# Kernel tuning notes

Hardware: AMD Instinct MI355X
Metric: run time of the kernel (lower is better)

## Reference

```python
import jax, jax.numpy as jnp
import numpy as np

M1, M2 = 20, 20  # retained DCT modes per layer

def dct1_last(x):
    # scipy.fftpack unnormalized DCT-I along last axis via FFT of even extension
    N = x.shape[-1]
    ext = jnp.concatenate([x, x[..., -2:0:-1]], axis=-1)  # length 2N-2
    return jnp.fft.rfft(ext).real[..., :N]

def dct1_2d(x):
    x = dct1_last(x)                       # along axis -1
    x = dct1_last(x.swapaxes(-1, -2)).swapaxes(-1, -2)  # along axis -2
    return x

def setup_inputs() -> dict:
    key = jax.random.key(0)
    ks = jax.random.split(key, 11)
    B, X, Y, Din, C, FC, Dout, L = 8, 256, 256, 3, 64, 128, 1, 3
    scale = 1.0 / (C * C)
    return {
        "x": jax.random.normal(ks[0], (B, X, Y, Din), jnp.float32),
        "fc0_w": jax.random.normal(ks[1], (Din, C), jnp.float32) * 0.1,
        "fc0_b": jax.random.normal(ks[2], (C,), jnp.float32) * 0.1,
        "sp_w1": scale * jax.random.uniform(ks[3], (L, C, C, M1, M2), jnp.float32),
        "sp_w2": scale * jax.random.uniform(ks[4], (L, C, C, M1, M2), jnp.float32),
        "conv_w": jax.random.normal(ks[5], (L, C, C), jnp.float32) * 0.05,
        "conv_b": jax.random.normal(ks[6], (L, C), jnp.float32) * 0.05,
        "fc1_w": jax.random.normal(ks[7], (C, FC), jnp.float32) * 0.05,
        "fc1_b": jax.random.normal(ks[8], (FC,), jnp.float32) * 0.05,
        "fc2_w": jax.random.normal(ks[9], (FC, Dout), jnp.float32) * 0.05,
        "fc2_b": jax.random.normal(ks[10], (Dout,), jnp.float32) * 0.05,
    }

def reference(x, fc0_w, fc0_b, sp_w1, sp_w2, conv_w, conv_b, fc1_w, fc1_b, fc2_w, fc2_b):
    h = x @ fc0_w + fc0_b                  # (B, X, Y, C)
    h = h.transpose(0, 3, 1, 2)            # (B, C, X, Y)
    B, C, X, Y = h.shape
    n_layers = sp_w1.shape[0]
    for i in range(n_layers):
        hd = dct1_2d(h)                    # forward DCT-I (unnormalized)
        # spectral mode multiply, scattered into zero spectrum (imag part is 0)
        out = jnp.zeros((B, C, X, Y), h.dtype)
        out = out.at[:, :, :M1, :M2].set(
            jnp.einsum('bixy,ioxy->boxy', hd[:, :, :M1, :M2], sp_w1[i]))
        out = out.at[:, :, X - M1:, :M2].set(
            jnp.einsum('bixy,ioxy->boxy', hd[:, :, X - M1:, :M2], sp_w2[i]))
        x1 = dct1_2d(out)                  # fftpack idct type-1 == dct type-1 (unnormalized)
        x2 = jnp.einsum('bixy,oi->boxy', h, conv_w[i]) + conv_b[i][None, :, None, None]
        h = x1 + x2
        if i != n_layers - 1:
            h = jnp.tanh(h)
    h = h.transpose(0, 2, 3, 1)            # (B, X, Y, C)
    h = jnp.tanh(h @ fc1_w + fc1_b)
    return h @ fc2_w + fc2_b               # (B, X, Y, 1)
```

## Files before the change

### kernel.cpp

```cpp
#include <hip/hip_runtime.h>
#include <math.h>

#define BB    8
#define CC    64
#define NN    256
#define MM    20
#define NKK   40
#define NLAY  3
#define FCD   128
#define PLANE (NN*NN)

__device__ __forceinline__ float fast_tanh(float x) {
    float xc = fminf(fmaxf(x, -15.f), 15.f);
    float e = __expf(2.f * xc);
    return (e - 1.f) / (e + 1.f);
}

__global__ __launch_bounds__(256) void k_basis(float* __restrict__ FlT, float* __restrict__ FkT,
                                               float* __restrict__ BkT, float* __restrict__ BlT,
                                               float* __restrict__ CwT, const float* __restrict__ conv_w) {
    int t = threadIdx.x;
    const double PI = 3.14159265358979323846;
    for (int j = t; j < NN*MM; j += 256) {
        int y = j / MM, l = j % MM;
        double g = (y == 0 || y == NN-1) ? 1.0 : 2.0;
        FlT[j] = (float)(g * cos(PI * (double)(l*y) / (double)(NN-1)));
    }
    for (int j = t; j < NN*NKK; j += 256) {
        int x = j / NKK, k = j % NKK;
        int rk = (k < MM) ? k : (NN - NKK + k);
        double g = (x == 0 || x == NN-1) ? 1.0 : 2.0;
        FkT[j] = (float)(g * cos(PI * (double)(rk*x) / (double)(NN-1)));
    }
    for (int j = t; j < NKK*NN; j += 256) {
        int k = j / NN, p = j % NN;
        int rk = (k < MM) ? k : (NN - NKK + k);
        double g = (rk == 0 || rk == NN-1) ? 1.0 : 2.0;
        BkT[j] = (float)(g * cos(PI * (double)(rk*p) / (double)(NN-1)));
    }
    for (int j = t; j < MM*NN; j += 256) {
        int l = j / NN, q = j % NN;
        double g = (l == 0) ? 1.0 : 2.0;
        BlT[j] = (float)(g * cos(PI * (double)(q*l) / (double)(NN-1)));
    }
    for (int j = t; j < NLAY*CC*CC; j += 256) {
        int lay = j / (CC*CC), r = j % (CC*CC);
        int i = r / CC, o = r % CC;
        CwT[j] = conv_w[lay*CC*CC + o*CC + i];
    }
}

__global__ __launch_bounds__(256) void k_fc0(const float* __restrict__ xin, const float* __restrict__ w,
                                             const float* __restrict__ bias, float* __restrict__ h) {
    __shared__ float xs[NN*3];
    int b = blockIdx.x >> 8, p = blockIdx.x & 255, q = threadIdx.x;
    size_t rowbase = ((size_t)(b*NN + p)*NN) * 3;
    for (int j = q; j < NN*3; j += 256) xs[j] = xin[rowbase + j];
    __syncthreads();
    float v0 = xs[q*3+0], v1 = xs[q*3+1], v2 = xs[q*3+2];
    size_t obase = (size_t)b*CC*PLANE + (size_t)p*NN + q;
    #pragma unroll 8
    for (int c = 0; c < CC; ++c) {
        float hv = bias[c] + v0*w[c] + v1*w[CC+c] + v2*w[2*CC+c];
        h[obase + (size_t)c*PLANE] = hv;
    }
}

__global__ __launch_bounds__(256, 2) void k_fwd(const float* __restrict__ h, const float* __restrict__ FkT,
                                                const float* __restrict__ FlT, float* __restrict__ Gt) {
    __shared__ float P[NKK][NN+1];
    int plane = blockIdx.x;
    int t = threadIdx.x;
    const float* hp = h + (size_t)plane * PLANE;
    float acc[NKK];
    #pragma unroll
    for (int k = 0; k < NKK; ++k) acc[k] = 0.f;
    #pragma unroll 2
    for (int x = 0; x < NN; ++x) {
        float hv = hp[x*NN + t];
        const float* fr = &FkT[x*NKK];
        #pragma unroll
        for (int k = 0; k < NKK; ++k) acc[k] += fr[k] * hv;
    }
    #pragma unroll
    for (int k = 0; k < NKK; ++k) P[k][t] = acc[k];
    __syncthreads();
    int b = plane >> 6, c = plane & 63;
    for (int j = t; j < NKK*MM; j += 256) {
        int k = j / MM, l = j % MM;
        float a = 0.f;
        for (int y = 0; y < NN; ++y) a += P[k][y] * FlT[y*MM + l];
        Gt[((size_t)(k*BB + b)*CC + c)*MM + l] = a;
    }
}

__global__ __launch_bounds__(256, 2) void k_spec(const float* __restrict__ Gt, const float* __restrict__ w1,
                                                 const float* __restrict__ w2, float* __restrict__ S) {
    extern __shared__ float gl[];
    int kb = blockIdx.x;
    int t = threadIdx.x;
    const float* chunk = Gt + (size_t)kb * (BB*CC*MM);
    for (int j = t; j < BB*CC*MM; j += 256) gl[j] = chunk[j];
    __syncthreads();
    int o = t & 63, g = t >> 6;
    int b0 = 2*g, b1 = 2*g + 1;
    const float* wp; int kk;
    if (kb < MM) { wp = w1; kk = kb; } else { wp = w2; kk = kb - MM; }
    float a0[MM], a1[MM];
    #pragma unroll
    for (int l = 0; l < MM; ++l) { a0[l] = 0.f; a1[l] = 0.f; }
    for (int i = 0; i < CC; ++i) {
        const float4* wr4 = reinterpret_cast<const float4*>(wp + ((size_t)(i*CC + o)*MM + kk)*MM);
        const float4* g04 = reinterpret_cast<const float4*>(&gl[(b0*CC + i)*MM]);
        const float4* g14 = reinterpret_cast<const float4*>(&gl[(b1*CC + i)*MM]);
        #pragma unroll
        for (int l4 = 0; l4 < MM/4; ++l4) {
            float4 wv = wr4[l4];
            float4 gv0 = g04[l4];
            float4 gv1 = g14[l4];
            a0[4*l4+0] += wv.x*gv0.x; a0[4*l4+1] += wv.y*gv0.y;
            a0[4*l4+2] += wv.z*gv0.z; a0[4*l4+3] += wv.w*gv0.w;
            a1[4*l4+0] += wv.x*gv1.x; a1[4*l4+1] += wv.y*gv1.y;
            a1[4*l4+2] += wv.z*gv1.z; a1[4*l4+3] += wv.w*gv1.w;
        }
    }
    #pragma unroll
    for (int l = 0; l < MM; ++l) {
        S[((size_t)(b0*NKK + kb)*MM + l)*CC + o] = a0[l];
        S[((size_t)(b1*NKK + kb)*MM + l)*CC + o] = a1[l];
    }
}

__global__ __launch_bounds__(256, 2) void k_inv1(const float* __restrict__ S, const float* __restrict__ BkT,
                                                 float* __restrict__ U) {
    int b = blockIdx.x >> 8, p = blockIdx.x & 255;
    int o = threadIdx.x & 63, w = threadIdx.x >> 6;
    float acc[5];
    #pragma unroll
    for (int j = 0; j < 5; ++j) acc[j] = 0.f;
    for (int k = 0; k < NKK; ++k) {
        float bk = BkT[k*NN + p];
        const float* sb = S + ((size_t)(b*NKK + k)*MM + w)*CC + o;
        #pragma unroll
        for (int j = 0; j < 5; ++j) acc[j] += bk * sb[(size_t)(4*j)*CC];
    }
    float* ub = U + ((size_t)(b*NN + p)*MM + w)*CC + o;
    #pragma unroll
    for (int j = 0; j < 5; ++j) ub[(size_t)(4*j)*CC] = acc[j];
}

__global__ __launch_bounds__(256, 2) void k_combine(float* h, const float* __restrict__ U,
                                                    const float* __restrict__ BlT, const float* __restrict__ cwt,
                                                    const float* __restrict__ cb) {
    int b = blockIdx.x >> 8, p = blockIdx.x & 255;
    int q = threadIdx.x;
    float acc[CC];
    #pragma unroll
    for (int o = 0; o < CC; ++o) acc[o] = cb[o];
    float* hb = h + (size_t)b*CC*PLANE + (size_t)p*NN + q;
    #pragma unroll 4
    for (int i = 0; i < CC; ++i) {
        float hv = hb[(size_t)i*PLANE];
        const float* wr = &cwt[i*CC];
        #pragma unroll
        for (int o = 0; o < CC; ++o) acc[o] += wr[o]*hv;
    }
    const float* ub = U + ((size_t)(b*NN + p)*MM)*CC;
    #pragma unroll 2
    for (int l = 0; l < MM; ++l) {
        float blv = BlT[l*NN + q];
        const float* ur = ub + (size_t)l*CC;
        #pragma unroll
        for (int o = 0; o < CC; ++o) acc[o] += ur[o]*blv;
    }
    #pragma unroll
    for (int o = 0; o < CC; ++o) hb[(size_t)o*PLANE] = fast_tanh(acc[o]);
}

__global__ __launch_bounds__(256, 2) void k_combine_fc(const float* __restrict__ h, const float* __restrict__ U,
        const float* __restrict__ BlT, const float* __restrict__ cwt, const float* __restrict__ cb,
        const float* __restrict__ w1, const float* __restrict__ b1,
        const float* __restrict__ w2, const float* __restrict__ b2, float* __restrict__ out) {
    int b = blockIdx.x >> 8, p = blockIdx.x & 255;
    int q = threadIdx.x;
    float acc[CC];
    #pragma unroll
    for (int o = 0; o < CC; ++o) acc[o] = cb[o];
    const float* hb = h + (size_t)b*CC*PLANE + (size_t)p*NN + q;
    #pragma unroll 4
    for (int i = 0; i < CC; ++i) {
        float hv = hb[(size_t)i*PLANE];
        const float* wr = &cwt[i*CC];
        #pragma unroll
        for (int o = 0; o < CC; ++o) acc[o] += wr[o]*hv;
    }
    const float* ub = U + ((size_t)(b*NN + p)*MM)*CC;
    #pragma unroll 2
    for (int l = 0; l < MM; ++l) {
        float blv = BlT[l*NN + q];
        const float* ur = ub + (size_t)l*CC;
        #pragma unroll
        for (int o = 0; o < CC; ++o) acc[o] += ur[o]*blv;
    }
    float ov = b2[0];
    const int FCH = 8;
    for (int f0 = 0; f0 < FCD; f0 += FCH) {
        float a[FCH];
        #pragma unroll
        for (int f = 0; f < FCH; ++f) a[f] = b1[f0 + f];
        #pragma unroll
        for (int i = 0; i < CC; ++i) {
            float hv = acc[i];
            const float* wr = &w1[i*FCD + f0];
            #pragma unroll
            for (int f = 0; f < FCH; ++f) a[f] += hv*wr[f];
        }
        #pragma unroll
        for (int f = 0; f < FCH; ++f) ov += fast_tanh(a[f]) * w2[f0 + f];
    }
    out[(size_t)blockIdx.x*NN + q] = ov;
}

extern "C" void kernel_launch(void* const* d_in, const int* in_sizes, int n_in,
                              void* d_out, int out_size, void* d_ws, size_t ws_size,
                              hipStream_t stream) {
    const float* x      = (const float*)d_in[0];
    const float* fc0_w  = (const float*)d_in[1];
    const float* fc0_b  = (const float*)d_in[2];
    const float* sp_w1  = (const float*)d_in[3];
    const float* sp_w2  = (const float*)d_in[4];
    const float* conv_w = (const float*)d_in[5];
    const float* conv_b = (const float*)d_in[6];
    const float* fc1_w  = (const float*)d_in[7];
    const float* fc1_b  = (const float*)d_in[8];
    const float* fc2_w  = (const float*)d_in[9];
    const float* fc2_b  = (const float*)d_in[10];

    float* ws = (float*)d_ws;
    const size_t HSZ = (size_t)BB*CC*PLANE;
    float* hA  = ws;
    float* Gt  = hA + HSZ;
    float* S   = Gt + (size_t)NKK*BB*CC*MM;
    float* U   = S  + (size_t)BB*NKK*MM*CC;
    float* FlT = U  + (size_t)BB*NN*MM*CC;
    float* FkT = FlT + NN*MM;
    float* BkT = FkT + NN*NKK;
    float* BlT = BkT + NKK*NN;
    float* CwT = BlT + MM*NN;

    k_basis<<<1, 256, 0, stream>>>(FlT, FkT, BkT, BlT, CwT, conv_w);
    k_fc0<<<BB*NN, 256, 0, stream>>>(x, fc0_w, fc0_b, hA);

    for (int lay = 0; lay < NLAY; ++lay) {
        const float* w1 = sp_w1 + (size_t)lay*CC*CC*MM*MM;
        const float* w2 = sp_w2 + (size_t)lay*CC*CC*MM*MM;
        k_fwd<<<BB*CC, 256, 0, stream>>>(hA, FkT, FlT, Gt);
        k_spec<<<NKK, 256, BB*CC*MM*sizeof(float), stream>>>(Gt, w1, w2, S);
        k_inv1<<<BB*NN, 256, 0, stream>>>(S, BkT, U);
        if (lay != NLAY-1) {
            k_combine<<<BB*NN, 256, 0, stream>>>(
                hA, U, BlT, CwT + lay*CC*CC, conv_b + lay*CC);
        } else {
            k_combine_fc<<<BB*NN, 256, 0, stream>>>(
                hA, U, BlT, CwT + lay*CC*CC, conv_b + lay*CC,
                fc1_w, fc1_b, fc2_w, fc2_b, (float*)d_out);
        }
    }
}
```

Measured before the change: 1.059 ms.

## Fold last-layer conv and spectral projection into fc1 weights

Precomputes the product of the last layer's pointwise conv weights with fc1 weights (and fused bias), and projects the inverse-spectral U rows through fc1 in shared memory per block. The final kernel then accumulates fc1 pre-activations directly from h and the projected U, skipping the intermediate 64-channel combine. This cuts per-pixel FMA count, but h is reloaded from global once per 32-feature chunk, and each block adds a shared-memory precompute with a barrier.

```diff
diff --git a/kernel.cpp b/kernel.cpp
--- a/kernel.cpp
+++ b/kernel.cpp
@@ -177,46 +177,61 @@
     for (int o = 0; o < CC; ++o) hb[(size_t)o*PLANE] = fast_tanh(acc[o]);
 }
 
-__global__ __launch_bounds__(256, 2) void k_combine_fc(const float* __restrict__ h, const float* __restrict__ U,
-        const float* __restrict__ BlT, const float* __restrict__ cwt, const float* __restrict__ cb,
+__global__ __launch_bounds__(256) void k_fuse_w(const float* __restrict__ cwt, const float* __restrict__ cb,
         const float* __restrict__ w1, const float* __restrict__ b1,
+        float* __restrict__ Wt, float* __restrict__ bt) {
+    int idx = blockIdx.x*256 + threadIdx.x;
+    int j = idx >> 7, f = idx & 127;
+    float s = 0.f;
+    #pragma unroll 8
+    for (int i = 0; i < CC; ++i) s += cwt[j*CC + i] * w1[i*FCD + f];
+    Wt[idx] = s;
+    if (idx < FCD) {
+        float sb = b1[idx];
+        for (int i = 0; i < CC; ++i) sb += cb[i] * w1[i*FCD + idx];
+        bt[idx] = sb;
+    }
+}
+
+__global__ __launch_bounds__(256, 2) void k_fc_last(const float* __restrict__ h, const float* __restrict__ U,
+        const float* __restrict__ BlT, const float* __restrict__ w1,
+        const float* __restrict__ Wt, const float* __restrict__ bt,
         const float* __restrict__ w2, const float* __restrict__ b2, float* __restrict__ out) {
+    __shared__ float ul[MM*FCD];
     int b = blockIdx.x >> 8, p = blockIdx.x & 255;
     int q = threadIdx.x;
-    float acc[CC];
-    #pragma unroll
-    for (int o = 0; o < CC; ++o) acc[o] = cb[o];
+    const float* ub = U + ((size_t)(b*NN + p)*MM)*CC;
+    for (int idx = q; idx < MM*FCD; idx += 256) {
+        int l = idx >> 7, f = idx & 127;
+        const float* ur = ub + l*CC;
+        float s = 0.f;
+        #pragma unroll 8
+        for (int o = 0; o < CC; ++o) s += ur[o] * w1[o*FCD + f];
+        ul[idx] = s;
+    }
+    __syncthreads();
     const float* hb = h + (size_t)b*CC*PLANE + (size_t)p*NN + q;
-    #pragma unroll 4
-    for (int i = 0; i < CC; ++i) {
-        float hv = hb[(size_t)i*PLANE];
-        const float* wr = &cwt[i*CC];
-        #pragma unroll
-        for (int o = 0; o < CC; ++o) acc[o] += wr[o]*hv;
-    }
-    const float* ub = U + ((size_t)(b*NN + p)*MM)*CC;
-    #pragma unroll 2
-    for (int l = 0; l < MM; ++l) {
-        float blv = BlT[l*NN + q];
-        const float* ur = ub + (size_t)l*CC;
-        #pragma unroll
-        for (int o = 0; o < CC; ++o) acc[o] += ur[o]*blv;
-    }
     float ov = b2[0];
-    const int FCH = 8;
-    for (int f0 = 0; f0 < FCD; f0 += FCH) {
-        float a[FCH];
-        #pragma unroll
-        for (int f = 0; f < FCH; ++f) a[f] = b1[f0 + f];
-        #pragma unroll
-        for (int i = 0; i < CC; ++i) {
-            float hv = acc[i];
-            const float* wr = &w1[i*FCD + f0];
+    for (int f0 = 0; f0 < FCD; f0 += 32) {
+        float a[32];
+        #pragma unroll
+        for (int f = 0; f < 32; ++f) a[f] = bt[f0 + f];
+        #pragma unroll 4
+        for (int j = 0; j < CC; ++j) {
+            float hv = hb[(size_t)j*PLANE];
+            const float* wr = &Wt[j*FCD + f0];
             #pragma unroll
-            for (int f = 0; f < FCH; ++f) a[f] += hv*wr[f];
-        }
-        #pragma unroll
-        for (int f = 0; f < FCH; ++f) ov += fast_tanh(a[f]) * w2[f0 + f];
+            for (int f = 0; f < 32; ++f) a[f] += hv*wr[f];
+        }
+        #pragma unroll 2
+        for (int l = 0; l < MM; ++l) {
+            float blv = BlT[l*NN + q];
+            const float* ur = &ul[l*FCD + f0];
+            #pragma unroll
+            for (int f = 0; f < 32; ++f) a[f] += blv*ur[f];
+        }
+        #pragma unroll
+        for (int f = 0; f < 32; ++f) ov += fast_tanh(a[f]) * w2[f0 + f];
     }
     out[(size_t)blockIdx.x*NN + q] = ov;
 }
@@ -247,9 +262,13 @@
     float* BkT = FkT + NN*NKK;
     float* BlT = BkT + NKK*NN;
     float* CwT = BlT + MM*NN;
+    float* Wt  = CwT + NLAY*CC*CC;
+    float* bt  = Wt  + CC*FCD;
 
     k_basis<<<1, 256, 0, stream>>>(FlT, FkT, BkT, BlT, CwT, conv_w);
     k_fc0<<<BB*NN, 256, 0, stream>>>(x, fc0_w, fc0_b, hA);
+    k_fuse_w<<<CC*FCD/256, 256, 0, stream>>>(CwT + (NLAY-1)*CC*CC, conv_b + (NLAY-1)*CC,
+                                             fc1_w, fc1_b, Wt, bt);
 
     for (int lay = 0; lay < NLAY; ++lay) {
         const float* w1 = sp_w1 + (size_t)lay*CC*CC*MM*MM;
@@ -261,9 +280,8 @@
             k_combine<<<BB*NN, 256, 0, stream>>>(
                 hA, U, BlT, CwT + lay*CC*CC, conv_b + lay*CC);
         } else {
-            k_combine_fc<<<BB*NN, 256, 0, stream>>>(
-                hA, U, BlT, CwT + lay*CC*CC, conv_b + lay*CC,
-                fc1_w, fc1_b, fc2_w, fc2_b, (float*)d_out);
-        }
-    }
-}
+            k_fc_last<<<BB*NN, 256, 0, stream>>>(
+                hA, U, BlT, fc1_w, Wt, bt, fc2_w, fc2_b, (float*)d_out);
+        }
+    }
+}
```

New measurement: 1.068 ms. No clear change (+0.9%).

## Split forward-DCT and combine kernels across more blocks with fewer registers

Applied to the files above, without the earlier changes.

k_fwd now launches two blocks per plane, each computing 20 of the 40 x-direction modes, which halves the accumulator array and shared buffer. k_combine now spreads each row over four blocks of 64 columns, with each wave producing 16 of the 64 output channels. A block barrier before the in-place write keeps all waves' reads of h ahead of the overwrite. This is meant to reduce register pressure and raise occupancy and block count. The cost is that h is read twice as often in k_fwd and is re-read by each wave in k_combine.

```diff
diff --git a/kernel.cpp b/kernel.cpp
--- a/kernel.cpp
+++ b/kernel.cpp
@@ -66,31 +66,33 @@
     }
 }
 
-__global__ __launch_bounds__(256, 2) void k_fwd(const float* __restrict__ h, const float* __restrict__ FkT,
+__global__ __launch_bounds__(256, 4) void k_fwd(const float* __restrict__ h, const float* __restrict__ FkT,
                                                 const float* __restrict__ FlT, float* __restrict__ Gt) {
-    __shared__ float P[NKK][NN+1];
-    int plane = blockIdx.x;
+    __shared__ float P[MM][NN+1];
+    int plane = blockIdx.x >> 1;
+    int g = blockIdx.x & 1;
     int t = threadIdx.x;
     const float* hp = h + (size_t)plane * PLANE;
-    float acc[NKK];
-    #pragma unroll
-    for (int k = 0; k < NKK; ++k) acc[k] = 0.f;
-    #pragma unroll 2
+    const float* fk = FkT + g*MM;
+    float acc[MM];
+    #pragma unroll
+    for (int k = 0; k < MM; ++k) acc[k] = 0.f;
+    #pragma unroll 4
     for (int x = 0; x < NN; ++x) {
         float hv = hp[x*NN + t];
-        const float* fr = &FkT[x*NKK];
-        #pragma unroll
-        for (int k = 0; k < NKK; ++k) acc[k] += fr[k] * hv;
-    }
-    #pragma unroll
-    for (int k = 0; k < NKK; ++k) P[k][t] = acc[k];
+        const float* fr = &fk[x*NKK];
+        #pragma unroll
+        for (int k = 0; k < MM; ++k) acc[k] += fr[k] * hv;
+    }
+    #pragma unroll
+    for (int k = 0; k < MM; ++k) P[k][t] = acc[k];
     __syncthreads();
     int b = plane >> 6, c = plane & 63;
-    for (int j = t; j < NKK*MM; j += 256) {
-        int k = j / MM, l = j % MM;
+    for (int j = t; j < MM*MM; j += 256) {
+        int kk = j / MM, l = j % MM;
         float a = 0.f;
-        for (int y = 0; y < NN; ++y) a += P[k][y] * FlT[y*MM + l];
-        Gt[((size_t)(k*BB + b)*CC + c)*MM + l] = a;
+        for (int y = 0; y < NN; ++y) a += P[kk][y] * FlT[y*MM + l];
+        Gt[((size_t)((g*MM + kk)*BB + b)*CC + c)*MM + l] = a;
     }
 }
 
@@ -149,32 +151,38 @@
     for (int j = 0; j < 5; ++j) ub[(size_t)(4*j)*CC] = acc[j];
 }
 
-__global__ __launch_bounds__(256, 2) void k_combine(float* h, const float* __restrict__ U,
+__global__ __launch_bounds__(256, 4) void k_combine(float* h, const float* __restrict__ U,
                                                     const float* __restrict__ BlT, const float* __restrict__ cwt,
                                                     const float* __restrict__ cb) {
-    int b = blockIdx.x >> 8, p = blockIdx.x & 255;
-    int q = threadIdx.x;
-    float acc[CC];
-    #pragma unroll
-    for (int o = 0; o < CC; ++o) acc[o] = cb[o];
+    int qc = blockIdx.x & 3;
+    int p  = (blockIdx.x >> 2) & 255;
+    int b  = blockIdx.x >> 10;
+    int lane = threadIdx.x & 63;
+    int w = __builtin_amdgcn_readfirstlane(threadIdx.x >> 6);
+    int q = qc*64 + lane;
+    int o0 = w*16;
+    float acc[16];
+    #pragma unroll
+    for (int oo = 0; oo < 16; ++oo) acc[oo] = cb[o0 + oo];
     float* hb = h + (size_t)b*CC*PLANE + (size_t)p*NN + q;
     #pragma unroll 4
     for (int i = 0; i < CC; ++i) {
         float hv = hb[(size_t)i*PLANE];
-        const float* wr = &cwt[i*CC];
-        #pragma unroll
-        for (int o = 0; o < CC; ++o) acc[o] += wr[o]*hv;
-    }
-    const float* ub = U + ((size_t)(b*NN + p)*MM)*CC;
-    #pragma unroll 2
+        const float* wr = &cwt[i*CC + o0];
+        #pragma unroll
+        for (int oo = 0; oo < 16; ++oo) acc[oo] += wr[oo]*hv;
+    }
+    const float* ub = U + ((size_t)(b*NN + p)*MM)*CC + o0;
+    #pragma unroll 4
     for (int l = 0; l < MM; ++l) {
         float blv = BlT[l*NN + q];
         const float* ur = ub + (size_t)l*CC;
         #pragma unroll
-        for (int o = 0; o < CC; ++o) acc[o] += ur[o]*blv;
-    }
-    #pragma unroll
-    for (int o = 0; o < CC; ++o) hb[(size_t)o*PLANE] = fast_tanh(acc[o]);
+        for (int oo = 0; oo < 16; ++oo) acc[oo] += ur[oo]*blv;
+    }
+    __syncthreads();
+    #pragma unroll
+    for (int oo = 0; oo < 16; ++oo) hb[(size_t)(o0 + oo)*PLANE] = fast_tanh(acc[oo]);
 }
 
 __global__ __launch_bounds__(256, 2) void k_combine_fc(const float* __restrict__ h, const float* __restrict__ U,
@@ -254,11 +262,11 @@
     for (int lay = 0; lay < NLAY; ++lay) {
         const float* w1 = sp_w1 + (size_t)lay*CC*CC*MM*MM;
         const float* w2 = sp_w2 + (size_t)lay*CC*CC*MM*MM;
-        k_fwd<<<BB*CC, 256, 0, stream>>>(hA, FkT, FlT, Gt);
+        k_fwd<<<BB*CC*2, 256, 0, stream>>>(hA, FkT, FlT, Gt);
         k_spec<<<NKK, 256, BB*CC*MM*sizeof(float), stream>>>(Gt, w1, w2, S);
         k_inv1<<<BB*NN, 256, 0, stream>>>(S, BkT, U);
         if (lay != NLAY-1) {
-            k_combine<<<BB*NN, 256, 0, stream>>>(
+            k_combine<<<BB*NN*4, 256, 0, stream>>>(
                 hA, U, BlT, CwT + lay*CC*CC, conv_b + lay*CC);
         } else {
             k_combine_fc<<<BB*NN, 256, 0, stream>>>(
```

Measured after the change: 993.3 us. -6.2%, faster.
